# Kernel tuning notes

Hardware: AMD Instinct MI355X
Metric: run time of the kernel (lower is better)

## Reference

```python
import jax, jax.numpy as jnp
import numpy as np

H, DK, D, DFF = 8, 64, 512, 512
B, S = 4, 1024
SCALE = 1.0 / np.sqrt(DK)


def _ln(x, g, b, eps=1e-5):
    m = jnp.mean(x, axis=-1, keepdims=True)
    v = jnp.mean((x - m) ** 2, axis=-1, keepdims=True)
    return (x - m) / jnp.sqrt(v + eps) * g + b


def _heads(x, w, b):
    bs, s, _ = x.shape
    return (x @ w + b).reshape(bs, s, H, DK).transpose(0, 2, 1, 3)  # [B,H,S,DK]


def _encoder_layer(x, qw, qb, kw, kb, vw, vb, ow, ob, g1, b1, w1, c1, w2, c2, g2, b2):
    # standard post-LN transformer encoder layer (sub_attention.Encoder(1))
    q = _heads(x, qw, qb)
    k = _heads(x, kw, kb)
    v = _heads(x, vw, vb)
    attn = jax.nn.softmax(jnp.einsum('bhqd,bhkd->bhqk', q, k) * SCALE, axis=-1)
    ctx = jnp.einsum('bhqk,bhkd->bhqd', attn, v).transpose(0, 2, 1, 3).reshape(x.shape[0], -1, H * DK)
    h = _ln(ctx @ ow + ob + x, g1, b1)
    f = jax.nn.relu(h @ w1 + c1) @ w2 + c2
    return _ln(f + h, g2, b2)


def setup_inputs() -> dict:
    key = jax.random.key(0)
    ks = iter(jax.random.split(key, 80))

    def nrm(*shape):
        return jax.random.normal(next(ks), shape, jnp.float32) * 0.02

    inp = {'audio_feat': jax.random.normal(next(ks), (B, S, D), jnp.float32),
           'video_feat': jax.random.normal(next(ks), (B, S, D), jnp.float32)}
    for p in ['aq', 'ak', 'av', 'vq', 'vk', 'vv', 'out']:
        inp[p + '_w'] = nrm(D, D)
        inp[p + '_b'] = jnp.zeros((D,), jnp.float32)
    inp['ln_g'] = jnp.ones((D,), jnp.float32)
    inp['ln_b'] = jnp.zeros((D,), jnp.float32)
    for pfx in ['asa_', 'vsa_']:
        for wn in ['qw', 'kw', 'vw', 'ow']:
            inp[pfx + wn] = nrm(D, D)
        for bn in ['qb', 'kb', 'vb', 'ob']:
            inp[pfx + bn] = jnp.zeros((D,), jnp.float32)
        inp[pfx + 'w1'] = nrm(D, DFF)
        inp[pfx + 'c1'] = jnp.zeros((DFF,), jnp.float32)
        inp[pfx + 'w2'] = nrm(DFF, D)
        inp[pfx + 'c2'] = jnp.zeros((D,), jnp.float32)
        inp[pfx + 'g1'] = jnp.ones((D,), jnp.float32)
        inp[pfx + 'b1'] = jnp.zeros((D,), jnp.float32)
        inp[pfx + 'g2'] = jnp.ones((D,), jnp.float32)
        inp[pfx + 'b2'] = jnp.zeros((D,), jnp.float32)
    return inp


def reference(audio_feat, video_feat, aq_w, aq_b, ak_w, ak_b, av_w, av_b, vq_w, vq_b, vk_w, vk_b, vv_w, vv_b, out_w, out_b, ln_g, ln_b, asa_qw, asa_qb, asa_kw, asa_kb, asa_vw, asa_vb, asa_ow, asa_ob, asa_g1, asa_b1, asa_w1, asa_c1, asa_w2, asa_c2, asa_g2, asa_b2, vsa_qw, vsa_qb, vsa_kw, vsa_kb, vsa_vw, vsa_vb, vsa_ow, vsa_ob, vsa_g1, vsa_b1, vsa_w1, vsa_c1, vsa_w2, vsa_c2, vsa_g2, vsa_b2):
    audio_self = _encoder_layer(audio_feat, asa_qw, asa_qb, asa_kw, asa_kb, asa_vw, asa_vb, asa_ow, asa_ob, asa_g1, asa_b1, asa_w1, asa_c1, asa_w2, asa_c2, asa_g2, asa_b2)
    video_self = _encoder_layer(video_feat, vsa_qw, vsa_qb, vsa_kw, vsa_kb, vsa_vw, vsa_vb, vsa_ow, vsa_ob, vsa_g1, vsa_b1, vsa_w1, vsa_c1, vsa_w2, vsa_c2, vsa_g2, vsa_b2)
    qa = _heads(audio_feat, aq_w, aq_b)
    ka = _heads(audio_feat, ak_w, ak_b)
    va = _heads(audio_feat, av_w, av_b)
    qv = _heads(video_feat, vq_w, vq_b)
    kv = _heads(video_feat, vk_w, vk_b)
    vvh = _heads(video_feat, vv_w, vv_b)
    attn_a = jax.nn.softmax(jnp.einsum('bhqd,bhkd->bhqk', qa, ka) * SCALE, axis=-1)
    attn_v = jax.nn.softmax(jnp.einsum('bhqd,bhkd->bhqk', qv, kv) * SCALE, axis=-1)
    attn = attn_a * attn_v  # dual-softmax elementwise combine
    ctx = jnp.einsum('bhqk,bhkd->bhqd', attn, va) * jnp.einsum('bhqk,bhkd->bhqd', attn, vvh)
    ctx = ctx.transpose(0, 2, 1, 3).reshape(audio_feat.shape[0], -1, H * DK)
    context = ctx @ out_w + out_b
    return _ln(audio_feat + context + audio_self + video_self, ln_g, ln_b)
```

## Files before the change

### kernel.cpp

```cpp
#include <hip/hip_runtime.h>
#include <cstddef>
#include <cstdint>


typedef __attribute__((ext_vector_type(8))) short s8v;
typedef __attribute__((ext_vector_type(4))) short s4v;
typedef __attribute__((ext_vector_type(4))) float f4v;

#define QSC 0.1803368801111444f
#define EXP2(x) __builtin_amdgcn_exp2f(x)
#define WAITV(N) asm volatile("s_waitcnt vmcnt(" #N ")" ::: "memory")
#define BAR() __builtin_amdgcn_s_barrier()

static __device__ __forceinline__ short f2bf(float f){
  unsigned int u = __builtin_bit_cast(unsigned int, f);
  u += 0x7fffu + ((u >> 16) & 1u);
  return (short)(u >> 16);
}
static __device__ __forceinline__ float bf2f(short s){
  unsigned int u = ((unsigned int)(unsigned short)s) << 16;
  return __builtin_bit_cast(float, u);
}
static __device__ __forceinline__ void gload16(const void* g, void* l){
  __builtin_amdgcn_global_load_lds(
      (const __attribute__((address_space(1))) unsigned int*)g,
      (__attribute__((address_space(3))) unsigned int*)l, 16, 0, 0);
}
#define MFMA16(a,b,c) __builtin_amdgcn_mfma_f32_16x16x32_bf16(a,b,c,0,0,0)

__global__ __launch_bounds__(256) void convert_in(const float* __restrict__ a,
                                                  const float* __restrict__ v,
                                                  short* __restrict__ oa,
                                                  short* __restrict__ ov){
  const float* src = blockIdx.y ? v : a;
  short* dst = blockIdx.y ? ov : oa;
  const int i = (blockIdx.x * 256 + threadIdx.x) * 8;
  float4 x = *reinterpret_cast<const float4*>(src + i);
  float4 y = *reinterpret_cast<const float4*>(src + i + 4);
  s8v o;
  o[0]=f2bf(x.x); o[1]=f2bf(x.y); o[2]=f2bf(x.z); o[3]=f2bf(x.w);
  o[4]=f2bf(y.x); o[5]=f2bf(y.y); o[6]=f2bf(y.z); o[7]=f2bf(y.w);
  *reinterpret_cast<s8v*>(dst + i) = o;
}

struct Ptr19 { const float* p[19]; };
__global__ __launch_bounds__(256) void pack_w(Ptr19 ws, short* __restrict__ wp){
  const int mat = blockIdx.y;
  const float* W = ws.p[mat];
  const int f = blockIdx.x * 256 + threadIdx.x;
  const int nblk = f >> 10, kg = (f >> 4) & 63, nl = f & 15;
  const int n = nblk * 16 + nl, k = kg * 8;
  s8v o;
#pragma unroll
  for (int e = 0; e < 8; ++e) o[e] = f2bf(W[(size_t)(k + e) * 512 + n]);
  *reinterpret_cast<s8v*>(wp + (size_t)mat * 262144 + (size_t)f * 8) = o;
}

struct GemmJobs { const short* A[12]; const short* W[12]; const float* bias[12];
                  short* C[12]; int mode[12]; };

__global__ __launch_bounds__(256, 2) void gemm_wide(GemmJobs J){
  int i = (blockIdx.z * 32 + blockIdx.y) * 2 + blockIdx.x;
  const int c = (64 * gridDim.z) >> 3;
  i = (i & 7) * c + (i >> 3);
  const int z = i >> 6, rem = i & 63;
  const int by = rem >> 1, bx = rem & 1;

  const short* __restrict__ A = J.A[z];
  const short* __restrict__ Wp = J.W[z];
  const float* __restrict__ bias = J.bias[z];
  short* __restrict__ C = J.C[z];
  const int md = J.mode[z];
  __shared__ short smem[32768];
  const int tid = threadIdx.x, lane = tid & 63, w = tid >> 6;
  const int wm = w >> 1, wn = w & 1;
  const int m0 = by * 128, n0 = bx * 256;
  const int lh = lane >> 4, ll = lane & 15;
  f4v acc[4][8] = {};

  auto stage = [&](int kt, int buf){
    const int k0 = kt * 32;
    short* As = smem + buf * 4096;
    short* Bs = smem + 8192 + buf * 8192;
#pragma unroll
    for (int p = 0; p < 2; ++p){
      const int f = tid + 256 * p;
      const int blk = f >> 6, kg = (f >> 4) & 3, il = f & 15;
      gload16(A + (size_t)(m0 + blk * 16 + il) * 512 + k0 + kg * 8, As + f * 8);
    }
#pragma unroll
    for (int p = 0; p < 4; ++p){
      const int f = tid + 256 * p;
      const int cblk = f >> 6, kg = (f >> 4) & 3, il = f & 15;
      gload16(Wp + ((size_t)(((n0 >> 4) + cblk) * 64 + (k0 >> 3) + kg) * 16 + il) * 8,
              Bs + f * 8);
    }
  };

  stage(0, 0);
#pragma unroll 1
  for (int kt = 0; kt < 16; ++kt){
    if (kt < 15) { stage(kt + 1, (kt + 1) & 1); WAITV(6); }
    else         { WAITV(0); }
    BAR();
    const int cur = kt & 1;
    const short* As = smem + cur * 4096;
    const short* Bs = smem + 8192 + cur * 8192;
    s8v a[4], b[8];
#pragma unroll
    for (int q = 0; q < 4; ++q)
      a[q] = *reinterpret_cast<const s8v*>(&As[(((wm*4+q)*4 + lh)*16 + ll) * 8]);
#pragma unroll
    for (int j = 0; j < 8; ++j)
      b[j] = *reinterpret_cast<const s8v*>(&Bs[(((wn*8+j)*4 + lh)*16 + ll) * 8]);
#pragma unroll
    for (int q = 0; q < 4; ++q)
#pragma unroll
      for (int j = 0; j < 8; ++j)
        acc[q][j] = MFMA16(a[q], b[j], acc[q][j]);
    BAR();
  }

  if (md == 2){
#pragma unroll
    for (int j = 0; j < 8; ++j){
      const int col = n0 + wn * 128 + j * 16 + ll;
      const float bv = bias[col];
      const int hh = col >> 6, dl = col & 63, dblk = dl >> 4, il = dl & 15;
#pragma unroll
      for (int q = 0; q < 4; ++q){
        const int rowb = m0 + wm * 64 + q * 16 + lh * 4;
        const int bb = rowb >> 10, srow = rowb & 1023;
        const size_t off = ((size_t)((bb*8 + hh)*16 + (srow >> 6))) * 4096
                         + (size_t)(((dblk << 7) + (((srow >> 3) & 7) << 4) + il) * 8 + (srow & 7));
        s4v o4;
#pragma unroll
        for (int r = 0; r < 4; ++r) o4[r] = f2bf(acc[q][j][r] + bv);
        *reinterpret_cast<s4v*>(&C[off]) = o4;
      }
    }
  } else {
    short* epi = smem + w * 8192;
    const float sc = (md == 1) ? QSC : 1.0f;
#pragma unroll
    for (int j = 0; j < 8; ++j){
      const float bv = bias[n0 + wn * 128 + j * 16 + ll];
#pragma unroll
      for (int q = 0; q < 4; ++q)
#pragma unroll
        for (int r = 0; r < 4; ++r)
          epi[(q*16 + lh*4 + r)*128 + j*16 + ll] = f2bf((acc[q][j][r] + bv) * sc);
    }
#pragma unroll
    for (int i2 = 0; i2 < 16; ++i2){
      const int row = i2 * 4 + (lane >> 4);
      s8v vr = *reinterpret_cast<const s8v*>(&epi[row*128 + (lane & 15)*8]);
      *reinterpret_cast<s8v*>(&C[(size_t)(m0 + wm*64 + row)*512 + n0 + wn*128 + (lane&15)*8]) = vr;
    }
  }
}

template<bool RELU>
__global__ __launch_bounds__(256) void gemm_n64(GemmJobs J){
  int i = (blockIdx.z * 32 + blockIdx.y) * 8 + blockIdx.x;
  const int c = (256 * gridDim.z) >> 3;
  i = (i & 7) * c + (i >> 3);
  const int z = i >> 8, rem = i & 255;
  const int by = rem >> 3, bx = rem & 7;

  const short* __restrict__ A = J.A[z];
  const short* __restrict__ Wp = J.W[z];
  const float* __restrict__ bias = J.bias[z];
  short* __restrict__ C = J.C[z];
  __shared__ short As[2][4096], Bs[2][2048];
  const int tid = threadIdx.x, lane = tid & 63, w = tid >> 6;
  const int wm = w >> 1, wn = w & 1;
  const int m0 = by * 128, n0 = bx * 64;
  const int lh = lane >> 4, ll = lane & 15;
  f4v acc[4][2] = {};

  auto stage = [&](int kt, int buf){
    const int k0 = kt * 32;
#pragma unroll
    for (int p = 0; p < 2; ++p){
      const int f = tid + 256 * p;
      const int blk = f >> 6, kg = (f >> 4) & 3, il = f & 15;
      gload16(A + (size_t)(m0 + blk * 16 + il) * 512 + k0 + kg * 8, &As[buf][f * 8]);
    }
    {
      const int f = tid;
      const int blk = f >> 6, kg = (f >> 4) & 3, il = f & 15;
      gload16(Wp + ((size_t)(((n0 >> 4) + blk) * 64 + (k0 >> 3) + kg) * 16 + il) * 8,
              &Bs[buf][f * 8]);
    }
  };

  stage(0, 0);
#pragma unroll
  for (int kt = 0; kt < 16; ++kt){
    if (kt < 15) { stage(kt + 1, (kt + 1) & 1); WAITV(3); }
    else         { WAITV(0); }
    BAR();
    const int cur = kt & 1;
    s8v a[4], b[2];
#pragma unroll
    for (int q = 0; q < 4; ++q)
      a[q] = *reinterpret_cast<const s8v*>(&As[cur][(((wm*4+q)*4 + lh)*16 + ll) * 8]);
#pragma unroll
    for (int j = 0; j < 2; ++j)
      b[j] = *reinterpret_cast<const s8v*>(&Bs[cur][(((wn*2+j)*4 + lh)*16 + ll) * 8]);
#pragma unroll
    for (int q = 0; q < 4; ++q)
#pragma unroll
      for (int j = 0; j < 2; ++j)
        acc[q][j] = MFMA16(a[q], b[j], acc[q][j]);
    BAR();
  }

  short* epi = &As[0][0] + w * 2048;
#pragma unroll
  for (int j = 0; j < 2; ++j){
    const float bv = bias[n0 + wn * 32 + j * 16 + ll];
#pragma unroll
    for (int q = 0; q < 4; ++q)
#pragma unroll
      for (int r = 0; r < 4; ++r){
        float v = acc[q][j][r] + bv;
        if (RELU) v = fmaxf(v, 0.f);
        epi[(q*16 + lh*4 + r)*32 + j*16 + ll] = f2bf(v);
      }
  }
#pragma unroll
  for (int i2 = 0; i2 < 4; ++i2){
    const int row = i2 * 16 + (lane >> 2);
    s8v vr = *reinterpret_cast<const s8v*>(&epi[row*32 + (lane & 3)*8]);
    *reinterpret_cast<s8v*>(&C[(size_t)(m0 + wm*64 + row)*512 + n0 + wn*32 + (lane&3)*8]) = vr;
  }
}

struct AttnJob { const short* Q; const short* K; const short* Vp; short* O; };

__global__ __launch_bounds__(512) void attn_enc(AttnJob j0, AttnJob j1){
  const AttnJob jb = blockIdx.z ? j1 : j0;
  __shared__ short KT[2][4096], VT[2][4096];
  __shared__ short PL[8][1024];
  const int tid = threadIdx.x, lane = tid & 63, w = tid >> 6;
  int bi = blockIdx.y * 8 + blockIdx.x;
  bi = (bi & 7) * 32 + (bi >> 3);
  const int qt = bi & 7, bh = bi >> 3;
  const int b = bh >> 3, h = bh & 7;
  const int q0 = qt * 128;
  const size_t base = (size_t)b * 1024 * 512 + (size_t)h * 64;
  const int lh = lane >> 4, ll = lane & 15;
  short* PLw = PL[w];

  s8v qf[2];
#pragma unroll
  for (int df = 0; df < 2; ++df)
    qf[df] = *reinterpret_cast<const s8v*>(jb.Q + base + (size_t)(q0 + w*16 + ll)*512 + lh*8 + df*32);

  const int sblk = tid >> 7, sg8 = (tid >> 4) & 7, sil = tid & 15;
  auto stage = [&](int it, int buf){
    gload16(jb.K + base + (size_t)(it*64 + sblk*16 + sil)*512 + sg8*8, &KT[buf][tid*8]);
    gload16(jb.Vp + ((size_t)bh*16 + it)*4096 + (size_t)tid*8, &VT[buf][tid*8]);
  };

  f4v o[4] = {};
  float zacc = 0.f;
  const int pwo = ((lh >> 1) * 16 + ll) * 8 + (lh & 1) * 4;
  const int pro = ((lh) * 16 + ll) * 8;

  stage(0, 0);
#pragma unroll 1
  for (int it = 0; it < 16; ++it){
    if (it < 15) { stage(it + 1, (it + 1) & 1); WAITV(2); }
    else         { WAITV(0); }
    BAR();
    const int cur = it & 1;

    f4v s[4] = {};
#pragma unroll
    for (int fn = 0; fn < 4; ++fn)
#pragma unroll
      for (int df = 0; df < 2; ++df){
        s8v kf = *reinterpret_cast<const s8v*>(&KT[cur][((fn*8 + lh + df*4)*16 + ll) * 8]);
        s[fn] = MFMA16(kf, qf[df], s[fn]);
      }

#pragma unroll
    for (int fn = 0; fn < 4; ++fn){
      s4v p4;
#pragma unroll
      for (int r = 0; r < 4; ++r){
        const float p = EXP2(s[fn][r]);
        zacc += p;
        p4[r] = f2bf(p);
      }
      *reinterpret_cast<s4v*>(&PLw[fn*256 + pwo]) = p4;
    }
    s8v pa[2];
#pragma unroll
    for (int kf2 = 0; kf2 < 2; ++kf2)
      pa[kf2] = *reinterpret_cast<const s8v*>(&PLw[kf2*512 + pro]);
#pragma unroll
    for (int fd = 0; fd < 4; ++fd)
#pragma unroll
      for (int kf2 = 0; kf2 < 2; ++kf2){
        s8v vf = *reinterpret_cast<const s8v*>(&VT[cur][((fd*8 + lh + kf2*4)*16 + ll) * 8]);
        o[fd] = MFMA16(vf, pa[kf2], o[fd]);
      }
    BAR();
  }

  float Z = zacc;
  Z += __shfl_xor(Z, 16); Z += __shfl_xor(Z, 32);
  const float rz = 1.f / Z;
#pragma unroll
  for (int fd = 0; fd < 4; ++fd){
    s4v o4;
#pragma unroll
    for (int r = 0; r < 4; ++r) o4[r] = f2bf(o[fd][r] * rz);
    *reinterpret_cast<s4v*>(&jb.O[base + (size_t)(q0 + w*16 + ll)*512 + fd*16 + lh*4]) = o4;
  }
}

__global__ __launch_bounds__(512) void attn_dual(const short* __restrict__ Qa, const short* __restrict__ Ka,
                                                 const short* __restrict__ Vap, const short* __restrict__ Qv,
                                                 const short* __restrict__ Kv, const short* __restrict__ Vvp,
                                                 short* __restrict__ O){
  __shared__ short KTa[2][4096], KTv[2][4096], VTa[2][4096], VTv[2][4096];
  __shared__ short PL[8][1024];
  const int tid = threadIdx.x, lane = tid & 63, w = tid >> 6;
  int bi = blockIdx.y * 8 + blockIdx.x;
  bi = (bi & 7) * 32 + (bi >> 3);
  const int qt = bi & 7, bh = bi >> 3;
  const int b = bh >> 3, h = bh & 7;
  const int q0 = qt * 128;
  const size_t base = (size_t)b * 1024 * 512 + (size_t)h * 64;
  const int lh = lane >> 4, ll = lane & 15;
  short* PLw = PL[w];

  s8v qfa[2], qfv[2];
#pragma unroll
  for (int df = 0; df < 2; ++df){
    const size_t ro = base + (size_t)(q0 + w*16 + ll)*512 + lh*8 + df*32;
    qfa[df] = *reinterpret_cast<const s8v*>(Qa + ro);
    qfv[df] = *reinterpret_cast<const s8v*>(Qv + ro);
  }

  const int sblk = tid >> 7, sg8 = (tid >> 4) & 7, sil = tid & 15;
  auto stage = [&](int it, int buf){
    const size_t krow = base + (size_t)(it*64 + sblk*16 + sil)*512 + sg8*8;
    gload16(Ka + krow, &KTa[buf][tid*8]);
    gload16(Kv + krow, &KTv[buf][tid*8]);
    const size_t voff = ((size_t)bh*16 + it)*4096 + (size_t)tid*8;
    gload16(Vap + voff, &VTa[buf][tid*8]);
    gload16(Vvp + voff, &VTv[buf][tid*8]);
  };

  f4v oa[4] = {}, ov[4] = {};
  float za = 0.f, zv = 0.f;
  const int pwo = ((lh >> 1) * 16 + ll) * 8 + (lh & 1) * 4;
  const int pro = ((lh) * 16 + ll) * 8;

  stage(0, 0);
#pragma unroll 1
  for (int it = 0; it < 16; ++it){
    if (it < 15) { stage(it + 1, (it + 1) & 1); WAITV(4); }
    else         { WAITV(0); }
    BAR();
    const int cur = it & 1;

    f4v sa[4] = {}, sv[4] = {};
#pragma unroll
    for (int fn = 0; fn < 4; ++fn)
#pragma unroll
      for (int df = 0; df < 2; ++df){
        const int boff = ((fn*8 + lh + df*4)*16 + ll) * 8;
        s8v ka = *reinterpret_cast<const s8v*>(&KTa[cur][boff]);
        s8v kv = *reinterpret_cast<const s8v*>(&KTv[cur][boff]);
        sa[fn] = MFMA16(ka, qfa[df], sa[fn]);
        sv[fn] = MFMA16(kv, qfv[df], sv[fn]);
      }

#pragma unroll
    for (int fn = 0; fn < 4; ++fn){
      s4v p4;
#pragma unroll
      for (int r = 0; r < 4; ++r){
        const float ea = EXP2(sa[fn][r]);
        const float ev = EXP2(sv[fn][r]);
        za += ea; zv += ev;
        p4[r] = f2bf(ea * ev);
      }
      *reinterpret_cast<s4v*>(&PLw[fn*256 + pwo]) = p4;
    }
    s8v pa[2];
#pragma unroll
    for (int kf2 = 0; kf2 < 2; ++kf2)
      pa[kf2] = *reinterpret_cast<const s8v*>(&PLw[kf2*512 + pro]);
#pragma unroll
    for (int fd = 0; fd < 4; ++fd)
#pragma unroll
      for (int kf2 = 0; kf2 < 2; ++kf2){
        const int boff = ((fd*8 + lh + kf2*4)*16 + ll) * 8;
        s8v va = *reinterpret_cast<const s8v*>(&VTa[cur][boff]);
        s8v vv = *reinterpret_cast<const s8v*>(&VTv[cur][boff]);
        oa[fd] = MFMA16(va, pa[kf2], oa[fd]);
        ov[fd] = MFMA16(vv, pa[kf2], ov[fd]);
      }
    BAR();
  }

  float Za = za, Zv = zv;
  Za += __shfl_xor(Za, 16); Za += __shfl_xor(Za, 32);
  Zv += __shfl_xor(Zv, 16); Zv += __shfl_xor(Zv, 32);
  const float rz = 1.f / (Za * Zv);
#pragma unroll
  for (int fd = 0; fd < 4; ++fd){
    s4v o4;
#pragma unroll
    for (int r = 0; r < 4; ++r){
      const float v = (oa[fd][r] * rz) * (ov[fd][r] * rz);
      o4[r] = f2bf(v);
    }
    *reinterpret_cast<s4v*>(&O[base + (size_t)(q0 + w*16 + ll)*512 + fd*16 + lh*4]) = o4;
  }
}

struct LnJob { const short* xb0; const short* xb1; const short* xb2;
               const float* xf; const float* g; const float* bb; void* out; };

template<int NBF, bool ADDF32, bool OUTF32>
__global__ __launch_bounds__(256) void ln_fused(LnJob j0, LnJob j1){
  const LnJob j = blockIdx.y ? j1 : j0;
  const int row = blockIdx.x, t = threadIdx.x;
  const size_t base = (size_t)row * 512;
  float x[2];
#pragma unroll
  for (int u = 0; u < 2; ++u){
    const int c = t + u * 256;
    float v = bf2f(j.xb0[base + c]);
    if (NBF > 1) v += bf2f(j.xb1[base + c]);
    if (NBF > 2) v += bf2f(j.xb2[base + c]);
    if (ADDF32) v += j.xf[base + c];
    x[u] = v;
  }
  float s = x[0] + x[1], ss = x[0]*x[0] + x[1]*x[1];
#pragma unroll
  for (int o = 32; o; o >>= 1){ s += __shfl_xor(s, o); ss += __shfl_xor(ss, o); }
  __shared__ float rb[8];
  const int wv = t >> 6;
  if ((t & 63) == 0){ rb[wv] = s; rb[wv + 4] = ss; }
  __syncthreads();
  s  = rb[0] + rb[1] + rb[2] + rb[3];
  ss = rb[4] + rb[5] + rb[6] + rb[7];
  const float m = s * (1.f / 512.f);
  const float var = ss * (1.f / 512.f) - m * m;
  const float rstd = rsqrtf(var + 1e-5f);
#pragma unroll
  for (int u = 0; u < 2; ++u){
    const int c = t + u * 256;
    const float v = (x[u] - m) * rstd * j.g[c] + j.bb[c];
    if (OUTF32) ((float*)j.out)[base + c] = v;
    else        ((short*)j.out)[base + c] = f2bf(v);
  }
}

__global__ __launch_bounds__(256) void ln_final(const short* __restrict__ fa, const short* __restrict__ ha,
                                                const short* __restrict__ fv, const short* __restrict__ hv,
                                                const short* __restrict__ ctx, const float* __restrict__ audio,
                                                const float* __restrict__ g2a, const float* __restrict__ b2a,
                                                const float* __restrict__ g2v, const float* __restrict__ b2v,
                                                const float* __restrict__ gf, const float* __restrict__ bf,
                                                float* __restrict__ out){
  const int row = blockIdx.x, t = threadIdx.x;
  const size_t base = (size_t)row * 512;
  __shared__ float rb[24];
  const int wv = t >> 6;

  auto reduce2 = [&](float a, float b, int p){
    float s = a + b, ss = a*a + b*b;
#pragma unroll
    for (int o = 32; o; o >>= 1){ s += __shfl_xor(s, o); ss += __shfl_xor(ss, o); }
    if ((t & 63) == 0){ rb[p*8 + wv] = s; rb[p*8 + 4 + wv] = ss; }
  };
  auto stats = [&](int p, float& m, float& rstd){
    const float s  = rb[p*8+0] + rb[p*8+1] + rb[p*8+2] + rb[p*8+3];
    const float ss = rb[p*8+4] + rb[p*8+5] + rb[p*8+6] + rb[p*8+7];
    m = s * (1.f / 512.f);
    rstd = rsqrtf(ss * (1.f / 512.f) - m * m + 1e-5f);
  };

  float xa[2], xv[2];
#pragma unroll
  for (int u = 0; u < 2; ++u){
    const int c = t + u * 256;
    xa[u] = bf2f(fa[base + c]) + bf2f(ha[base + c]);
    xv[u] = bf2f(fv[base + c]) + bf2f(hv[base + c]);
  }
  reduce2(xa[0], xa[1], 0);
  reduce2(xv[0], xv[1], 1);
  __syncthreads();
  float ma, ra, mv, rv;
  stats(0, ma, ra);
  stats(1, mv, rv);

  float xf[2];
#pragma unroll
  for (int u = 0; u < 2; ++u){
    const int c = t + u * 256;
    const float sa = (xa[u] - ma) * ra * g2a[c] + b2a[c];
    const float sv = (xv[u] - mv) * rv * g2v[c] + b2v[c];
    xf[u] = audio[base + c] + bf2f(ctx[base + c]) + sa + sv;
  }
  reduce2(xf[0], xf[1], 2);
  __syncthreads();
  float mf, rf;
  stats(2, mf, rf);
#pragma unroll
  for (int u = 0; u < 2; ++u){
    const int c = t + u * 256;
    out[base + c] = (xf[u] - mf) * rf * gf[c] + bf[c];
  }
}

extern "C" void kernel_launch(void* const* d_in, const int* in_sizes, int n_in,
                              void* d_out, int out_size, void* d_ws, size_t ws_size,
                              hipStream_t stream) {
  const float* audio = (const float*)d_in[0];
  const float* video = (const float*)d_in[1];
  auto F = [&](int i){ return (const float*)d_in[i]; };

  short* ws16 = (short*)d_ws;
  const size_t SL = 2097152;
  auto S = [&](int i){ return ws16 + (size_t)i * SL; };
  short* Wp = S(12);
  auto WP = [&](int i){ return (const short*)(Wp + (size_t)i * 262144); };
  short* Kcv = (short*)d_out;
  short* Vcv = (short*)d_out + SL;

  convert_in<<<dim3(1024,2), 256, 0, stream>>>(audio, video, S(10), S(11));

  Ptr19 pw;
  const int widx[19] = {18,19,20,21,26,28, 34,35,36,37,42,44, 2,4,6,8,10,12, 14};
  for (int i = 0; i < 19; ++i) pw.p[i] = F(widx[i]);
  pack_w<<<dim3(128,19), 256, 0, stream>>>(pw, Wp);

  GemmJobs g1{};
  const short* g1A[12] = {S(10),S(10),S(10), S(11),S(11),S(11), S(10),S(10),S(10), S(11),S(11),S(11)};
  const short* g1W[12] = {WP(0),WP(1),WP(2), WP(6),WP(7),WP(8), WP(12),WP(13),WP(14), WP(15),WP(16),WP(17)};
  const float* g1B[12] = {F(22),F(23),F(24), F(38),F(39),F(40), F(3),F(5),F(7), F(9),F(11),F(13)};
  short*       g1C[12] = {S(0),S(1),S(2), S(3),S(4),S(5), S(6),S(7),S(8), S(9),Kcv,Vcv};
  const int    g1M[12] = {1,0,2, 1,0,2, 1,0,2, 1,0,2};
  for (int i = 0; i < 12; ++i){ g1.A[i]=g1A[i]; g1.W[i]=g1W[i]; g1.bias[i]=g1B[i]; g1.C[i]=g1C[i]; g1.mode[i]=g1M[i]; }
  gemm_wide<<<dim3(2,32,12), 256, 0, stream>>>(g1);

  attn_enc<<<dim3(8,32,2), 512, 0, stream>>>(AttnJob{S(0),S(1),S(2),S(10)},
                                             AttnJob{S(3),S(4),S(5),S(11)});

  attn_dual<<<dim3(8,32), 512, 0, stream>>>(S(6),S(7),S(8), S(9),Kcv,Vcv, S(0));

  GemmJobs g39{};
  g39.A[0]=S(10); g39.W[0]=WP(3);  g39.bias[0]=F(25); g39.C[0]=S(1); g39.mode[0]=0;
  g39.A[1]=S(11); g39.W[1]=WP(9);  g39.bias[1]=F(41); g39.C[1]=S(2); g39.mode[1]=0;
  g39.A[2]=S(0);  g39.W[2]=WP(18); g39.bias[2]=F(15); g39.C[2]=S(3); g39.mode[2]=0;
  gemm_n64<false><<<dim3(8,32,3), 256, 0, stream>>>(g39);

  ln_fused<1,true,false><<<dim3(4096,2), 256, 0, stream>>>(
      LnJob{S(1),nullptr,nullptr, audio, F(30),F(31), S(4)},
      LnJob{S(2),nullptr,nullptr, video, F(46),F(47), S(5)});

  GemmJobs g5{};
  g5.A[0]=S(4); g5.W[0]=WP(4);  g5.bias[0]=F(27); g5.C[0]=S(6); g5.mode[0]=0;
  g5.A[1]=S(5); g5.W[1]=WP(10); g5.bias[1]=F(43); g5.C[1]=S(7); g5.mode[1]=0;
  gemm_n64<true><<<dim3(8,32,2), 256, 0, stream>>>(g5);

  GemmJobs g6{};
  g6.A[0]=S(6); g6.W[0]=WP(5);  g6.bias[0]=F(29); g6.C[0]=S(8); g6.mode[0]=0;
  g6.A[1]=S(7); g6.W[1]=WP(11); g6.bias[1]=F(45); g6.C[1]=S(9); g6.mode[1]=0;
  gemm_n64<false><<<dim3(8,32,2), 256, 0, stream>>>(g6);

  ln_final<<<4096, 256, 0, stream>>>(S(8),S(4), S(9),S(5), S(3), audio,
                                     F(32),F(33), F(48),F(49), F(16),F(17),
                                     (float*)d_out);
}
```

Measured before the change: 176.4 us.

## Triple-buffer GEMM LDS pipeline and merge input conversion with weight packing

Both GEMM kernels move from double to triple LDS buffering with a prefetch distance of two k-tiles. This lets them drop the trailing barrier each iteration, so there is one barrier per k-step instead of two. The input bf16 conversion and weight packing kernels are merged into one launch to save a kernel launch and let the two jobs run at the same time. The extra LDS (72KB in gemm_wide) may limit occupancy under the 2-block launch bound, and the wait counts must stay correct for the deeper prefetch.

```diff
diff --git a/kernel.cpp b/kernel.cpp
--- a/kernel.cpp
+++ b/kernel.cpp
@@ -28,32 +28,36 @@
 }
 #define MFMA16(a,b,c) __builtin_amdgcn_mfma_f32_16x16x32_bf16(a,b,c,0,0,0)
 
-__global__ __launch_bounds__(256) void convert_in(const float* __restrict__ a,
-                                                  const float* __restrict__ v,
-                                                  short* __restrict__ oa,
-                                                  short* __restrict__ ov){
-  const float* src = blockIdx.y ? v : a;
-  short* dst = blockIdx.y ? ov : oa;
-  const int i = (blockIdx.x * 256 + threadIdx.x) * 8;
-  float4 x = *reinterpret_cast<const float4*>(src + i);
-  float4 y = *reinterpret_cast<const float4*>(src + i + 4);
-  s8v o;
-  o[0]=f2bf(x.x); o[1]=f2bf(x.y); o[2]=f2bf(x.z); o[3]=f2bf(x.w);
-  o[4]=f2bf(y.x); o[5]=f2bf(y.y); o[6]=f2bf(y.z); o[7]=f2bf(y.w);
-  *reinterpret_cast<s8v*>(dst + i) = o;
-}
-
 struct Ptr19 { const float* p[19]; };
-__global__ __launch_bounds__(256) void pack_w(Ptr19 ws, short* __restrict__ wp){
-  const int mat = blockIdx.y;
-  const float* W = ws.p[mat];
-  const int f = blockIdx.x * 256 + threadIdx.x;
-  const int nblk = f >> 10, kg = (f >> 4) & 63, nl = f & 15;
-  const int n = nblk * 16 + nl, k = kg * 8;
-  s8v o;
-#pragma unroll
-  for (int e = 0; e < 8; ++e) o[e] = f2bf(W[(size_t)(k + e) * 512 + n]);
-  *reinterpret_cast<s8v*>(wp + (size_t)mat * 262144 + (size_t)f * 8) = o;
+
+__global__ __launch_bounds__(256) void prep(const float* __restrict__ a,
+                                            const float* __restrict__ v,
+                                            short* __restrict__ oa,
+                                            short* __restrict__ ov,
+                                            Ptr19 ws, short* __restrict__ wp){
+  const int b = blockIdx.x, tid = threadIdx.x;
+  if (b < 2048){
+    const float* src = (b >= 1024) ? v : a;
+    short* dst = (b >= 1024) ? ov : oa;
+    const int i = ((b & 1023) * 256 + tid) * 8;
+    float4 x = *reinterpret_cast<const float4*>(src + i);
+    float4 y = *reinterpret_cast<const float4*>(src + i + 4);
+    s8v o;
+    o[0]=f2bf(x.x); o[1]=f2bf(x.y); o[2]=f2bf(x.z); o[3]=f2bf(x.w);
+    o[4]=f2bf(y.x); o[5]=f2bf(y.y); o[6]=f2bf(y.z); o[7]=f2bf(y.w);
+    *reinterpret_cast<s8v*>(dst + i) = o;
+  } else {
+    const int pb = b - 2048;
+    const int mat = pb >> 7;
+    const float* W = ws.p[mat];
+    const int f = (pb & 127) * 256 + tid;
+    const int nblk = f >> 10, kg = (f >> 4) & 63, nl = f & 15;
+    const int n = nblk * 16 + nl, k = kg * 8;
+    s8v o;
+#pragma unroll
+    for (int e = 0; e < 8; ++e) o[e] = f2bf(W[(size_t)(k + e) * 512 + n]);
+    *reinterpret_cast<s8v*>(wp + (size_t)mat * 262144 + (size_t)f * 8) = o;
+  }
 }
 
 struct GemmJobs { const short* A[12]; const short* W[12]; const float* bias[12];
@@ -71,7 +75,7 @@
   const float* __restrict__ bias = J.bias[z];
   short* __restrict__ C = J.C[z];
   const int md = J.mode[z];
-  __shared__ short smem[32768];
+  __shared__ short smem[36864];
   const int tid = threadIdx.x, lane = tid & 63, w = tid >> 6;
   const int wm = w >> 1, wn = w & 1;
   const int m0 = by * 128, n0 = bx * 256;
@@ -81,7 +85,7 @@
   auto stage = [&](int kt, int buf){
     const int k0 = kt * 32;
     short* As = smem + buf * 4096;
-    short* Bs = smem + 8192 + buf * 8192;
+    short* Bs = smem + 12288 + buf * 8192;
 #pragma unroll
     for (int p = 0; p < 2; ++p){
       const int f = tid + 256 * p;
@@ -98,14 +102,15 @@
   };
 
   stage(0, 0);
+  stage(1, 1);
 #pragma unroll 1
   for (int kt = 0; kt < 16; ++kt){
-    if (kt < 15) { stage(kt + 1, (kt + 1) & 1); WAITV(6); }
-    else         { WAITV(0); }
+    if (kt < 15) { WAITV(6); } else { WAITV(0); }
     BAR();
-    const int cur = kt & 1;
+    if (kt < 14) stage(kt + 2, (kt + 2) % 3);
+    const int cur = kt % 3;
     const short* As = smem + cur * 4096;
-    const short* Bs = smem + 8192 + cur * 8192;
+    const short* Bs = smem + 12288 + cur * 8192;
     s8v a[4], b[8];
 #pragma unroll
     for (int q = 0; q < 4; ++q)
@@ -118,8 +123,8 @@
 #pragma unroll
       for (int j = 0; j < 8; ++j)
         acc[q][j] = MFMA16(a[q], b[j], acc[q][j]);
-    BAR();
-  }
+  }
+  BAR();
 
   if (md == 2){
 #pragma unroll
@@ -172,7 +177,7 @@
   const short* __restrict__ Wp = J.W[z];
   const float* __restrict__ bias = J.bias[z];
   short* __restrict__ C = J.C[z];
-  __shared__ short As[2][4096], Bs[2][2048];
+  __shared__ short As[3][4096], Bs[3][2048];
   const int tid = threadIdx.x, lane = tid & 63, w = tid >> 6;
   const int wm = w >> 1, wn = w & 1;
   const int m0 = by * 128, n0 = bx * 64;
@@ -196,12 +201,13 @@
   };
 
   stage(0, 0);
-#pragma unroll
+  stage(1, 1);
+#pragma unroll 1
   for (int kt = 0; kt < 16; ++kt){
-    if (kt < 15) { stage(kt + 1, (kt + 1) & 1); WAITV(3); }
-    else         { WAITV(0); }
+    if (kt < 15) { WAITV(3); } else { WAITV(0); }
     BAR();
-    const int cur = kt & 1;
+    if (kt < 14) stage(kt + 2, (kt + 2) % 3);
+    const int cur = kt % 3;
     s8v a[4], b[2];
 #pragma unroll
     for (int q = 0; q < 4; ++q)
@@ -214,8 +220,8 @@
 #pragma unroll
       for (int j = 0; j < 2; ++j)
         acc[q][j] = MFMA16(a[q], b[j], acc[q][j]);
-    BAR();
-  }
+  }
+  BAR();
 
   short* epi = &As[0][0] + w * 2048;
 #pragma unroll
@@ -540,12 +546,10 @@
   short* Kcv = (short*)d_out;
   short* Vcv = (short*)d_out + SL;
 
-  convert_in<<<dim3(1024,2), 256, 0, stream>>>(audio, video, S(10), S(11));
-
   Ptr19 pw;
   const int widx[19] = {18,19,20,21,26,28, 34,35,36,37,42,44, 2,4,6,8,10,12, 14};
   for (int i = 0; i < 19; ++i) pw.p[i] = F(widx[i]);
-  pack_w<<<dim3(128,19), 256, 0, stream>>>(pw, Wp);
+  prep<<<4480, 256, 0, stream>>>(audio, video, S(10), S(11), pw, Wp);
 
   GemmJobs g1{};
   const short* g1A[12] = {S(10),S(10),S(10), S(11),S(11),S(11), S(10),S(10),S(10), S(11),S(11),S(11)};
```

After: 176.4 us. No clear change (+0.0%).
